# Optimization experiments

Hardware: AMD Instinct MI355X
Metric: run time of the kernel (lower is better)

Reference implementation:

```python
import jax, jax.numpy as jnp
import numpy as np

C = 16        # channel_n
HID = 128     # hidden width of 1x1 MLP
FIRE_RATE = 0.5
STEP_SIZE = 1.0
ALIVE_THRESH = 0.1
B, H, W = 16, 256, 256


def _perceive_kernel():
    # identity + Sobel filters, angle = 0.0 so cos=1, sin=0
    ident = np.outer([0.0, 1.0, 0.0], [0.0, 1.0, 0.0]).astype(np.float32)
    dxk = (np.outer([1.0, 2.0, 1.0], [-1.0, 0.0, 1.0]) / 8.0).astype(np.float32)
    dyk = dxk.T
    k3 = np.stack([ident, dxk, dyk], axis=-1)  # [3,3,3]
    # TF depthwise layout: out channel index = c*3 + k  -> tile over channels
    rhs = np.tile(k3, (1, 1, C)).reshape(3, 3, 1, 3 * C)  # HWIO, groups=C
    return jnp.asarray(rhs)


def _get_living_mask(x):
    alpha = x[:, :, :, 3:4]
    pooled = jax.lax.reduce_window(alpha, -jnp.inf, jax.lax.max,
                                   (1, 3, 3, 1), (1, 1, 1, 1), 'SAME')
    return pooled > ALIVE_THRESH


def _perceive(x):
    rhs = _perceive_kernel()
    return jax.lax.conv_general_dilated(
        x, rhs, window_strides=(1, 1), padding='SAME',
        dimension_numbers=('NHWC', 'HWIO', 'NHWC'),
        feature_group_count=C)  # [B,H,W,3C]


def setup_inputs() -> dict:
    key = jax.random.key(0)
    kx, kw1, kb1, ku = jax.random.split(key, 4)
    x = jax.random.normal(kx, (B, H, W, C), dtype=jnp.float32)
    # dmodel params: Conv2D(128,1,relu) then Conv2D(16,1,zeros init); use
    # random values for a meaningful numeric baseline
    W1 = jax.random.normal(kw1, (3 * C, HID), dtype=jnp.float32) * 0.1
    b1 = jax.random.normal(kb1, (HID,), dtype=jnp.float32) * 0.01
    W2 = jax.random.normal(jax.random.fold_in(key, 7), (HID, C), dtype=jnp.float32) * 0.1
    b2 = jnp.zeros((C,), dtype=jnp.float32)
    rand_u = jax.random.uniform(ku, (B, H, W, 1), dtype=jnp.float32)
    return {"x": x, "W1": W1, "b1": b1, "W2": W2, "b2": b2, "rand_u": rand_u}


def reference(x, W1, b1, W2, b2, rand_u):
    pre_life_mask = _get_living_mask(x)
    y = _perceive(x)                                         # [B,H,W,48]
    h = jax.nn.relu(jnp.einsum('bhwc,cd->bhwd', y, W1) + b1)  # [B,H,W,128]
    dx = (jnp.einsum('bhwd,dc->bhwc', h, W2) + b2) * STEP_SIZE
    update_mask = (rand_u <= FIRE_RATE).astype(x.dtype)
    x = x + dx * update_mask
    post_life_mask = _get_living_mask(x)
    life_mask = (pre_life_mask & post_life_mask).astype(x.dtype)
    return x * life_mask
```

## Files before the change

### kernel.cpp

```cpp
#include <hip/hip_runtime.h>


#define NB 16
#define NH 256
#define NW 256
#define NC 16
#define NHID 128
#define NPIX (NB*NH*NW)

__global__ __launch_bounds__(256) void ca_update(
    const float* __restrict__ x, const float* __restrict__ W1,
    const float* __restrict__ b1, const float* __restrict__ W2,
    const float* __restrict__ b2, const float* __restrict__ rand_u,
    float* __restrict__ out, float* __restrict__ ws_alpha, float* __restrict__ ws_pre)
{
    __shared__ float tile[18 * 18 * 17];

    const int tid = threadIdx.x;
    const int w0 = blockIdx.x * 16;
    const int h0 = blockIdx.y * 16;
    const int bb = blockIdx.z;

    for (int i = tid; i < 18 * 18; i += 256) {
        const int ly = i / 18, lx = i - ly * 18;
        const int gh = h0 + ly - 1, gw = w0 + lx - 1;
        float4 v0, v1, v2, v3;
        if (gh >= 0 && gh < NH && gw >= 0 && gw < NW) {
            const float4* p = (const float4*)(x + (((size_t)bb * NH + gh) * NW + gw) * NC);
            v0 = p[0]; v1 = p[1]; v2 = p[2]; v3 = p[3];
        } else {
            v0 = v1 = v2 = v3 = make_float4(0.f, 0.f, 0.f, 0.f);
        }
        float* t = &tile[i * 17];
        t[0]=v0.x; t[1]=v0.y; t[2]=v0.z; t[3]=v0.w;
        t[4]=v1.x; t[5]=v1.y; t[6]=v1.z; t[7]=v1.w;
        t[8]=v2.x; t[9]=v2.y; t[10]=v2.z; t[11]=v2.w;
        t[12]=v3.x; t[13]=v3.y; t[14]=v3.z; t[15]=v3.w;
    }
    __syncthreads();

    const int tx = tid & 15, ty = tid >> 4;
    const int lcc = ((ty + 1) * 18 + (tx + 1)) * 17;
    const int lmm = (ty * 18 + tx) * 17;
    const int lm0 = (ty * 18 + tx + 1) * 17;
    const int lmp = (ty * 18 + tx + 2) * 17;
    const int l0m = ((ty + 1) * 18 + tx) * 17;
    const int l0p = ((ty + 1) * 18 + tx + 2) * 17;
    const int lpm = ((ty + 2) * 18 + tx) * 17;
    const int lp0 = ((ty + 2) * 18 + tx + 1) * 17;
    const int lpp = ((ty + 2) * 18 + tx + 2) * 17;

    float y[48];
    #pragma unroll
    for (int c = 0; c < NC; ++c) {
        const float xmm = tile[lmm + c], xm0 = tile[lm0 + c], xmp = tile[lmp + c];
        const float x0m = tile[l0m + c], xcc = tile[lcc + c], x0p = tile[l0p + c];
        const float xpm = tile[lpm + c], xp0 = tile[lp0 + c], xpp = tile[lpp + c];
        y[3*c + 0] = xcc;
        y[3*c + 1] = ((xmp - xmm) + 2.f * (x0p - x0m) + (xpp - xpm)) * 0.125f;
        y[3*c + 2] = ((xpm - xmm) + 2.f * (xp0 - xm0) + (xpp - xmp)) * 0.125f;
    }

    float am = tile[lmm + 3];
    am = fmaxf(am, tile[lm0 + 3]); am = fmaxf(am, tile[lmp + 3]);
    am = fmaxf(am, tile[l0m + 3]); am = fmaxf(am, tile[lcc + 3]);
    am = fmaxf(am, tile[l0p + 3]);
    am = fmaxf(am, tile[lpm + 3]); am = fmaxf(am, tile[lp0 + 3]);
    am = fmaxf(am, tile[lpp + 3]);
    const float pre = (am > 0.1f) ? 1.f : 0.f;

    float dxacc[NC];
    #pragma unroll
    for (int c = 0; c < NC; ++c) dxacc[c] = b2[c];

    for (int d0 = 0; d0 < NHID; d0 += 4) {
        float a0 = b1[d0 + 0], a1 = b1[d0 + 1], a2 = b1[d0 + 2], a3 = b1[d0 + 3];
        #pragma unroll
        for (int c = 0; c < 48; ++c) {
            const float* wp = &W1[c * NHID + d0];
            const float yc = y[c];
            a0 = fmaf(yc, wp[0], a0);
            a1 = fmaf(yc, wp[1], a1);
            a2 = fmaf(yc, wp[2], a2);
            a3 = fmaf(yc, wp[3], a3);
        }
        a0 = fmaxf(a0, 0.f); a1 = fmaxf(a1, 0.f);
        a2 = fmaxf(a2, 0.f); a3 = fmaxf(a3, 0.f);
        const float* w2p = &W2[d0 * NC];
        #pragma unroll
        for (int c = 0; c < NC; ++c) {
            float t = fmaf(a0, w2p[c], dxacc[c]);
            t = fmaf(a1, w2p[NC + c], t);
            t = fmaf(a2, w2p[2 * NC + c], t);
            dxacc[c] = fmaf(a3, w2p[3 * NC + c], t);
        }
    }

    const size_t pix = ((size_t)bb * NH + (h0 + ty)) * NW + (w0 + tx);
    const float um = (rand_u[pix] <= 0.5f) ? 1.f : 0.f;
    float nx[NC];
    #pragma unroll
    for (int c = 0; c < NC; ++c) nx[c] = fmaf(dxacc[c], um, tile[lcc + c]);

    float4* po = (float4*)(out + pix * NC);
    po[0] = make_float4(nx[0], nx[1], nx[2], nx[3]);
    po[1] = make_float4(nx[4], nx[5], nx[6], nx[7]);
    po[2] = make_float4(nx[8], nx[9], nx[10], nx[11]);
    po[3] = make_float4(nx[12], nx[13], nx[14], nx[15]);
    ws_alpha[pix] = nx[3];
    ws_pre[pix] = pre;
}

__global__ __launch_bounds__(256) void ca_mask(
    const float* __restrict__ ws_alpha, const float* __restrict__ ws_pre,
    float* __restrict__ out)
{
    const size_t pix = (size_t)blockIdx.x * 256 + threadIdx.x;
    const int w = (int)(pix & 255);
    const int h = (int)((pix >> 8) & 255);
    const size_t base = pix - w - ((size_t)h << 8);

    float m = -1e30f;
    #pragma unroll
    for (int dy = -1; dy <= 1; ++dy) {
        const int hh = h + dy;
        if (hh < 0 || hh >= NH) continue;
        const size_t row = base + (size_t)hh * NW;
        #pragma unroll
        for (int dw = -1; dw <= 1; ++dw) {
            const int ww = w + dw;
            if (ww < 0 || ww >= NW) continue;
            m = fmaxf(m, ws_alpha[row + ww]);
        }
    }
    const bool life = (ws_pre[pix] != 0.f) && (m > 0.1f);
    const float s = life ? 1.f : 0.f;

    float4* po = (float4*)(out + pix * NC);
    #pragma unroll
    for (int i = 0; i < 4; ++i) {
        float4 v = po[i];
        v.x *= s; v.y *= s; v.z *= s; v.w *= s;
        po[i] = v;
    }
}

extern "C" void kernel_launch(void* const* d_in, const int* in_sizes, int n_in,
                              void* d_out, int out_size, void* d_ws, size_t ws_size,
                              hipStream_t stream) {
    (void)in_sizes; (void)n_in; (void)out_size; (void)ws_size;
    const float* x      = (const float*)d_in[0];
    const float* W1     = (const float*)d_in[1];
    const float* b1     = (const float*)d_in[2];
    const float* W2     = (const float*)d_in[3];
    const float* b2     = (const float*)d_in[4];
    const float* rand_u = (const float*)d_in[5];
    float* out = (float*)d_out;
    float* ws_alpha = (float*)d_ws;
    float* ws_pre   = ws_alpha + NPIX;

    dim3 gridA(NW / 16, NH / 16, NB);
    ca_update<<<gridA, 256, 0, stream>>>(x, W1, b1, W2, b2, rand_u, out, ws_alpha, ws_pre);
    ca_mask<<<NPIX / 256, 256, 0, stream>>>(ws_alpha, ws_pre, out);
}
```

Before: 391.2 us.

## Run the per-pixel MLP on bf16 MFMA with an exact fp32 recheck near the alive threshold

```diff
diff --git a/kernel.cpp b/kernel.cpp
--- a/kernel.cpp
+++ b/kernel.cpp
@@ -1,147 +1,292 @@
 #include <hip/hip_runtime.h>
 
 
-#define NB 16
-#define NH 256
-#define NW 256
 #define NC 16
 #define NHID 128
-#define NPIX (NB*NH*NW)
-
-__global__ __launch_bounds__(256) void ca_update(
+#define NPIX (16 * 256 * 256)
+#define MG 0.015f
+
+typedef __attribute__((ext_vector_type(8))) short s8b;
+typedef __attribute__((ext_vector_type(4))) float f4;
+
+__device__ __forceinline__ unsigned short f2bf(float f) {
+    union { float f; unsigned int u; } v; v.f = f;
+    unsigned int r = (v.u + 0x7FFFu + ((v.u >> 16) & 1u)) >> 16;
+    return (unsigned short)r;
+}
+__device__ __forceinline__ unsigned int pack2(float a, float b) {
+    return (unsigned int)f2bf(a) | ((unsigned int)f2bf(b) << 16);
+}
+
+__global__ __launch_bounds__(256) void ca_prep(
+    const float* __restrict__ W1, const float* __restrict__ b1,
+    const float* __restrict__ W2, uint4* __restrict__ w1p, uint4* __restrict__ w2p)
+{
+    const int tid = threadIdx.x;
+    if (blockIdx.x == 0) {
+        for (int idx = tid; idx < 1024; idx += 256) {
+            const int fid = idx >> 6, lane = idx & 63;
+            const int k0 = fid >> 3, mt = fid & 7;
+            const int q = lane >> 4, i = lane & 15;
+            unsigned int u[4];
+            #pragma unroll
+            for (int jp = 0; jp < 4; ++jp) {
+                int k = k0 * 32 + q * 8 + jp * 2;
+                float v0 = (k < 48) ? W1[k * 128 + mt * 16 + i] : ((k == 48) ? b1[mt * 16 + i] : 0.f);
+                k++;
+                float v1 = (k < 48) ? W1[k * 128 + mt * 16 + i] : ((k == 48) ? b1[mt * 16 + i] : 0.f);
+                u[jp] = pack2(v0, v1);
+            }
+            w1p[idx] = make_uint4(u[0], u[1], u[2], u[3]);
+        }
+    } else {
+        for (int idx = tid; idx < 256; idx += 256) {
+            const int k2 = idx >> 6, lane = idx & 63;
+            const int q = lane >> 4, i = lane & 15;
+            unsigned int u[4];
+            #pragma unroll
+            for (int jp = 0; jp < 4; ++jp) {
+                const int k = k2 * 32 + q * 8 + jp * 2;
+                u[jp] = pack2(W2[k * 16 + i], W2[(k + 1) * 16 + i]);
+            }
+            w2p[idx] = make_uint4(u[0], u[1], u[2], u[3]);
+        }
+    }
+}
+
+__global__ __launch_bounds__(256, 2) void ca_update(
+    const float* __restrict__ x, const float* __restrict__ b2,
+    const float* __restrict__ rand_u, const uint4* __restrict__ w1p,
+    const uint4* __restrict__ w2p, float* __restrict__ out,
+    float* __restrict__ ws_alpha, unsigned char* __restrict__ ws_pre)
+{
+    __shared__ __align__(16) float xt[18 * 18 * 20];
+    __shared__ __align__(16) unsigned short yfs[4 * 2 * 528];
+    __shared__ __align__(16) unsigned short hbs[4 * 16 * 136];
+    __shared__ float lsr[256];
+
+    const int tid  = threadIdx.x;
+    const int lane = tid & 63;
+    const int li   = lane & 15;
+    const int lq   = lane >> 4;
+    const int wv   = tid >> 6;
+    const int tx   = tid & 15, ty = tid >> 4;
+    const int w0 = blockIdx.x * 16, h0 = blockIdx.y * 16, bb = blockIdx.z;
+
+    s8b w1f[2][8], w2f[4];
+    const s8b* w1s = (const s8b*)w1p;
+    const s8b* w2s = (const s8b*)w2p;
+    #pragma unroll
+    for (int k0 = 0; k0 < 2; ++k0)
+        #pragma unroll
+        for (int mt = 0; mt < 8; ++mt)
+            w1f[k0][mt] = w1s[(k0 * 8 + mt) * 64 + lane];
+    #pragma unroll
+    for (int k2 = 0; k2 < 4; ++k2) w2f[k2] = w2s[k2 * 64 + lane];
+    float b2v[4];
+    #pragma unroll
+    for (int r = 0; r < 4; ++r) b2v[r] = b2[lq * 4 + r];
+
+    for (int i = tid; i < 324; i += 256) {
+        const int ly = i / 18, lx = i - ly * 18;
+        const int gh = h0 + ly - 1, gw = w0 + lx - 1;
+        float4 v0, v1, v2, v3;
+        if (gh >= 0 && gh < 256 && gw >= 0 && gw < 256) {
+            const float4* p = (const float4*)(x + (((size_t)bb * 256 + gh) * 256 + gw) * NC);
+            v0 = p[0]; v1 = p[1]; v2 = p[2]; v3 = p[3];
+        } else {
+            v0 = v1 = v2 = v3 = make_float4(0.f, 0.f, 0.f, 0.f);
+        }
+        float4* t = (float4*)(xt + i * 20);
+        t[0] = v0; t[1] = v1; t[2] = v2; t[3] = v3;
+    }
+    const size_t gpix = ((size_t)bb * 256 + h0 + ty) * 256 + (w0 + tx);
+    lsr[tid] = rand_u[gpix];
+    __syncthreads();
+
+    const int o_mm = ((ty + 0) * 18 + tx + 0) * 20, o_m0 = ((ty + 0) * 18 + tx + 1) * 20, o_mp = ((ty + 0) * 18 + tx + 2) * 20;
+    const int o_0m = ((ty + 1) * 18 + tx + 0) * 20, o_cc = ((ty + 1) * 18 + tx + 1) * 20, o_0p = ((ty + 1) * 18 + tx + 2) * 20;
+    const int o_pm = ((ty + 2) * 18 + tx + 0) * 20, o_p0 = ((ty + 2) * 18 + tx + 1) * 20, o_pp = ((ty + 2) * 18 + tx + 2) * 20;
+
+    float am = xt[o_mm + 3];
+    am = fmaxf(am, xt[o_m0 + 3]); am = fmaxf(am, xt[o_mp + 3]);
+    am = fmaxf(am, xt[o_0m + 3]); am = fmaxf(am, xt[o_cc + 3]); am = fmaxf(am, xt[o_0p + 3]);
+    am = fmaxf(am, xt[o_pm + 3]); am = fmaxf(am, xt[o_p0 + 3]); am = fmaxf(am, xt[o_pp + 3]);
+    ws_pre[gpix] = (am > 0.1f) ? (unsigned char)1 : (unsigned char)0;
+
+    unsigned int yu[24];
+    #pragma unroll
+    for (int cq = 0; cq < 4; ++cq) {
+        const int co = cq * 4;
+        float4 vmm = *(const float4*)(xt + o_mm + co); const float* pmm = (const float*)&vmm;
+        float4 vm0 = *(const float4*)(xt + o_m0 + co); const float* pm0 = (const float*)&vm0;
+        float4 vmp = *(const float4*)(xt + o_mp + co); const float* pmp = (const float*)&vmp;
+        float4 v0m = *(const float4*)(xt + o_0m + co); const float* p0m = (const float*)&v0m;
+        float4 vcc = *(const float4*)(xt + o_cc + co); const float* pcc = (const float*)&vcc;
+        float4 v0p = *(const float4*)(xt + o_0p + co); const float* p0p = (const float*)&v0p;
+        float4 vpm = *(const float4*)(xt + o_pm + co); const float* ppm = (const float*)&vpm;
+        float4 vp0 = *(const float4*)(xt + o_p0 + co); const float* pp0 = (const float*)&vp0;
+        float4 vpp = *(const float4*)(xt + o_pp + co); const float* ppp = (const float*)&vpp;
+        float yl[12];
+        #pragma unroll
+        for (int cc = 0; cc < 4; ++cc) {
+            const float xmm = pmm[cc], xm0 = pm0[cc], xmp = pmp[cc];
+            const float x0m = p0m[cc], xcc = pcc[cc], x0p = p0p[cc];
+            const float xpm = ppm[cc], xp0 = pp0[cc], xpp = ppp[cc];
+            yl[cc * 3 + 0] = xcc;
+            yl[cc * 3 + 1] = ((xmp - xmm) + 2.f * (x0p - x0m) + (xpp - xpm)) * 0.125f;
+            yl[cc * 3 + 2] = ((xpm - xmm) + 2.f * (xp0 - xm0) + (xpp - xmp)) * 0.125f;
+        }
+        #pragma unroll
+        for (int m2 = 0; m2 < 6; ++m2) yu[cq * 6 + m2] = pack2(yl[2 * m2], yl[2 * m2 + 1]);
+    }
+
+    unsigned short* yfw = yfs + wv * (2 * 528);
+    unsigned short* hbw = hbs + wv * (16 * 136);
+
+    for (int s = 0; s < 4; ++s) {
+        const int t = wv * 4 + s;
+        if ((ty & 3) == s) {
+            #pragma unroll
+            for (int q = 0; q < 4; ++q)
+                *(uint4*)(yfw + (q * 16 + tx) * 8) = make_uint4(yu[q * 4], yu[q * 4 + 1], yu[q * 4 + 2], yu[q * 4 + 3]);
+            *(uint4*)(yfw + 528 + (0 * 16 + tx) * 8) = make_uint4(yu[16], yu[17], yu[18], yu[19]);
+            *(uint4*)(yfw + 528 + (1 * 16 + tx) * 8) = make_uint4(yu[20], yu[21], yu[22], yu[23]);
+            *(uint4*)(yfw + 528 + (2 * 16 + tx) * 8) = make_uint4(0x3F80u, 0u, 0u, 0u);
+            *(uint4*)(yfw + 528 + (3 * 16 + tx) * 8) = make_uint4(0u, 0u, 0u, 0u);
+        }
+        __syncthreads();
+        const s8b ya0 = *(const s8b*)(yfw + lane * 8);
+        const s8b ya1 = *(const s8b*)(yfw + 528 + lane * 8);
+        f4 acc1[8];
+        #pragma unroll
+        for (int mt = 0; mt < 8; ++mt) { f4 z = {0.f, 0.f, 0.f, 0.f}; acc1[mt] = z; }
+        #pragma unroll
+        for (int mt = 0; mt < 8; ++mt)
+            acc1[mt] = __builtin_amdgcn_mfma_f32_16x16x32_bf16(w1f[0][mt], ya0, acc1[mt], 0, 0, 0);
+        #pragma unroll
+        for (int mt = 0; mt < 8; ++mt)
+            acc1[mt] = __builtin_amdgcn_mfma_f32_16x16x32_bf16(w1f[1][mt], ya1, acc1[mt], 0, 0, 0);
+        #pragma unroll
+        for (int mt = 0; mt < 8; ++mt) {
+            const float hh0 = fmaxf(acc1[mt][0], 0.f), hh1 = fmaxf(acc1[mt][1], 0.f);
+            const float hh2 = fmaxf(acc1[mt][2], 0.f), hh3 = fmaxf(acc1[mt][3], 0.f);
+            *(uint2*)(hbw + li * 136 + mt * 16 + lq * 4) = make_uint2(pack2(hh0, hh1), pack2(hh2, hh3));
+        }
+        __syncthreads();
+        f4 acc2 = {0.f, 0.f, 0.f, 0.f};
+        #pragma unroll
+        for (int k2 = 0; k2 < 4; ++k2) {
+            const s8b hf = *(const s8b*)(hbw + li * 136 + k2 * 32 + lq * 8);
+            acc2 = __builtin_amdgcn_mfma_f32_16x16x32_bf16(w2f[k2], hf, acc2, 0, 0, 0);
+        }
+        const float um = (lsr[t * 16 + li] <= 0.5f) ? 1.f : 0.f;
+        const float4 xc = *(const float4*)(xt + ((t + 1) * 18 + li + 1) * 20 + lq * 4);
+        float4 nx;
+        nx.x = fmaf(acc2[0] + b2v[0], um, xc.x);
+        nx.y = fmaf(acc2[1] + b2v[1], um, xc.y);
+        nx.z = fmaf(acc2[2] + b2v[2], um, xc.z);
+        nx.w = fmaf(acc2[3] + b2v[3], um, xc.w);
+        const size_t gp = ((size_t)bb * 256 + h0 + t) * 256 + (w0 + li);
+        ((float4*)out)[gp * 4 + lq] = nx;
+        if (lq == 0) ws_alpha[gp] = nx.w;
+    }
+}
+
+__device__ float exact_alpha(
     const float* __restrict__ x, const float* __restrict__ W1,
     const float* __restrict__ b1, const float* __restrict__ W2,
     const float* __restrict__ b2, const float* __restrict__ rand_u,
-    float* __restrict__ out, float* __restrict__ ws_alpha, float* __restrict__ ws_pre)
+    int bb, int gh, int gw)
 {
-    __shared__ float tile[18 * 18 * 17];
-
+    const size_t p = ((size_t)bb * 256 + gh) * 256 + gw;
+    const float xa = x[p * 16 + 3];
+    if (rand_u[p] > 0.5f) return xa;
+    float y[48];
+    #pragma unroll
+    for (int k = 0; k < 48; ++k) y[k] = 0.f;
+    for (int dy = 0; dy < 3; ++dy) {
+        for (int dx = 0; dx < 3; ++dx) {
+            const int hh = gh + dy - 1, ww = gw + dx - 1;
+            if (hh < 0 || hh >= 256 || ww < 0 || ww >= 256) continue;
+            const float* f = x + (((size_t)bb * 256 + hh) * 256 + ww) * 16;
+            const float rw = (dy == 1) ? 2.f : 1.f;
+            const float cw = (dx == 1) ? 2.f : 1.f;
+            const float wx = rw * (float)(dx - 1) * 0.125f;
+            const float wy = cw * (float)(dy - 1) * 0.125f;
+            const bool ctr = (dy == 1 && dx == 1);
+            #pragma unroll
+            for (int c = 0; c < 16; ++c) {
+                const float v = f[c];
+                if (ctr) y[3 * c] = v;
+                y[3 * c + 1] = fmaf(v, wx, y[3 * c + 1]);
+                y[3 * c + 2] = fmaf(v, wy, y[3 * c + 2]);
+            }
+        }
+    }
+    float dot = b2[3];
+    for (int d4 = 0; d4 < 32; ++d4) {
+        const float4 a4 = *(const float4*)(b1 + d4 * 4);
+        float a0 = a4.x, a1 = a4.y, a2 = a4.z, a3 = a4.w;
+        for (int k = 0; k < 48; ++k) {
+            const float4 w = *(const float4*)(W1 + k * 128 + d4 * 4);
+            const float yk = y[k];
+            a0 = fmaf(yk, w.x, a0); a1 = fmaf(yk, w.y, a1);
+            a2 = fmaf(yk, w.z, a2); a3 = fmaf(yk, w.w, a3);
+        }
+        dot = fmaf(fmaxf(a0, 0.f), W2[(d4 * 4 + 0) * 16 + 3], dot);
+        dot = fmaf(fmaxf(a1, 0.f), W2[(d4 * 4 + 1) * 16 + 3], dot);
+        dot = fmaf(fmaxf(a2, 0.f), W2[(d4 * 4 + 2) * 16 + 3], dot);
+        dot = fmaf(fmaxf(a3, 0.f), W2[(d4 * 4 + 3) * 16 + 3], dot);
+    }
+    return xa + dot;
+}
+
+__global__ __launch_bounds__(256) void ca_mask(
+    const float* __restrict__ x, const float* __restrict__ W1,
+    const float* __restrict__ b1, const float* __restrict__ W2,
+    const float* __restrict__ b2, const float* __restrict__ rand_u,
+    const float* __restrict__ alpha, const unsigned char* __restrict__ pre,
+    float* __restrict__ out)
+{
+    __shared__ float at[18 * 20];
     const int tid = threadIdx.x;
-    const int w0 = blockIdx.x * 16;
-    const int h0 = blockIdx.y * 16;
-    const int bb = blockIdx.z;
-
-    for (int i = tid; i < 18 * 18; i += 256) {
+    const int w0 = blockIdx.x * 16, h0 = blockIdx.y * 16, bb = blockIdx.z;
+    for (int i = tid; i < 324; i += 256) {
         const int ly = i / 18, lx = i - ly * 18;
         const int gh = h0 + ly - 1, gw = w0 + lx - 1;
-        float4 v0, v1, v2, v3;
-        if (gh >= 0 && gh < NH && gw >= 0 && gw < NW) {
-            const float4* p = (const float4*)(x + (((size_t)bb * NH + gh) * NW + gw) * NC);
-            v0 = p[0]; v1 = p[1]; v2 = p[2]; v3 = p[3];
-        } else {
-            v0 = v1 = v2 = v3 = make_float4(0.f, 0.f, 0.f, 0.f);
-        }
-        float* t = &tile[i * 17];
-        t[0]=v0.x; t[1]=v0.y; t[2]=v0.z; t[3]=v0.w;
-        t[4]=v1.x; t[5]=v1.y; t[6]=v1.z; t[7]=v1.w;
-        t[8]=v2.x; t[9]=v2.y; t[10]=v2.z; t[11]=v2.w;
-        t[12]=v3.x; t[13]=v3.y; t[14]=v3.z; t[15]=v3.w;
+        float v = 0.f;
+        if (gh >= 0 && gh < 256 && gw >= 0 && gw < 256)
+            v = alpha[((size_t)bb * 256 + gh) * 256 + gw];
+        at[ly * 20 + lx] = v;
     }
     __syncthreads();
-
-    const int tx = tid & 15, ty = tid >> 4;
-    const int lcc = ((ty + 1) * 18 + (tx + 1)) * 17;
-    const int lmm = (ty * 18 + tx) * 17;
-    const int lm0 = (ty * 18 + tx + 1) * 17;
-    const int lmp = (ty * 18 + tx + 2) * 17;
-    const int l0m = ((ty + 1) * 18 + tx) * 17;
-    const int l0p = ((ty + 1) * 18 + tx + 2) * 17;
-    const int lpm = ((ty + 2) * 18 + tx) * 17;
-    const int lp0 = ((ty + 2) * 18 + tx + 1) * 17;
-    const int lpp = ((ty + 2) * 18 + tx + 2) * 17;
-
-    float y[48];
-    #pragma unroll
-    for (int c = 0; c < NC; ++c) {
-        const float xmm = tile[lmm + c], xm0 = tile[lm0 + c], xmp = tile[lmp + c];
-        const float x0m = tile[l0m + c], xcc = tile[lcc + c], x0p = tile[l0p + c];
-        const float xpm = tile[lpm + c], xp0 = tile[lp0 + c], xpp = tile[lpp + c];
-        y[3*c + 0] = xcc;
-        y[3*c + 1] = ((xmp - xmm) + 2.f * (x0p - x0m) + (xpp - xpm)) * 0.125f;
-        y[3*c + 2] = ((xpm - xmm) + 2.f * (xp0 - xm0) + (xpp - xmp)) * 0.125f;
-    }
-
-    float am = tile[lmm + 3];
-    am = fmaxf(am, tile[lm0 + 3]); am = fmaxf(am, tile[lmp + 3]);
-    am = fmaxf(am, tile[l0m + 3]); am = fmaxf(am, tile[lcc + 3]);
-    am = fmaxf(am, tile[l0p + 3]);
-    am = fmaxf(am, tile[lpm + 3]); am = fmaxf(am, tile[lp0 + 3]);
-    am = fmaxf(am, tile[lpp + 3]);
-    const float pre = (am > 0.1f) ? 1.f : 0.f;
-
-    float dxacc[NC];
-    #pragma unroll
-    for (int c = 0; c < NC; ++c) dxacc[c] = b2[c];
-
-    for (int d0 = 0; d0 < NHID; d0 += 4) {
-        float a0 = b1[d0 + 0], a1 = b1[d0 + 1], a2 = b1[d0 + 2], a3 = b1[d0 + 3];
-        #pragma unroll
-        for (int c = 0; c < 48; ++c) {
-            const float* wp = &W1[c * NHID + d0];
-            const float yc = y[c];
-            a0 = fmaf(yc, wp[0], a0);
-            a1 = fmaf(yc, wp[1], a1);
-            a2 = fmaf(yc, wp[2], a2);
-            a3 = fmaf(yc, wp[3], a3);
-        }
-        a0 = fmaxf(a0, 0.f); a1 = fmaxf(a1, 0.f);
-        a2 = fmaxf(a2, 0.f); a3 = fmaxf(a3, 0.f);
-        const float* w2p = &W2[d0 * NC];
-        #pragma unroll
-        for (int c = 0; c < NC; ++c) {
-            float t = fmaf(a0, w2p[c], dxacc[c]);
-            t = fmaf(a1, w2p[NC + c], t);
-            t = fmaf(a2, w2p[2 * NC + c], t);
-            dxacc[c] = fmaf(a3, w2p[3 * NC + c], t);
-        }
-    }
-
-    const size_t pix = ((size_t)bb * NH + (h0 + ty)) * NW + (w0 + tx);
-    const float um = (rand_u[pix] <= 0.5f) ? 1.f : 0.f;
-    float nx[NC];
-    #pragma unroll
-    for (int c = 0; c < NC; ++c) nx[c] = fmaf(dxacc[c], um, tile[lcc + c]);
-
-    float4* po = (float4*)(out + pix * NC);
-    po[0] = make_float4(nx[0], nx[1], nx[2], nx[3]);
-    po[1] = make_float4(nx[4], nx[5], nx[6], nx[7]);
-    po[2] = make_float4(nx[8], nx[9], nx[10], nx[11]);
-    po[3] = make_float4(nx[12], nx[13], nx[14], nx[15]);
-    ws_alpha[pix] = nx[3];
-    ws_pre[pix] = pre;
-}
-
-__global__ __launch_bounds__(256) void ca_mask(
-    const float* __restrict__ ws_alpha, const float* __restrict__ ws_pre,
-    float* __restrict__ out)
-{
-    const size_t pix = (size_t)blockIdx.x * 256 + threadIdx.x;
-    const int w = (int)(pix & 255);
-    const int h = (int)((pix >> 8) & 255);
-    const size_t base = pix - w - ((size_t)h << 8);
-
-    float m = -1e30f;
-    #pragma unroll
-    for (int dy = -1; dy <= 1; ++dy) {
-        const int hh = h + dy;
-        if (hh < 0 || hh >= NH) continue;
-        const size_t row = base + (size_t)hh * NW;
-        #pragma unroll
-        for (int dw = -1; dw <= 1; ++dw) {
-            const int ww = w + dw;
-            if (ww < 0 || ww >= NW) continue;
-            m = fmaxf(m, ws_alpha[row + ww]);
-        }
-    }
-    const bool life = (ws_pre[pix] != 0.f) && (m > 0.1f);
-    const float s = life ? 1.f : 0.f;
-
-    float4* po = (float4*)(out + pix * NC);
-    #pragma unroll
-    for (int i = 0; i < 4; ++i) {
-        float4 v = po[i];
-        v.x *= s; v.y *= s; v.z *= s; v.w *= s;
-        po[i] = v;
+    const int txx = tid & 15, tyy = tid >> 4;
+    float m = at[tyy * 20 + txx];
+    m = fmaxf(m, at[tyy * 20 + txx + 1]); m = fmaxf(m, at[tyy * 20 + txx + 2]);
+    m = fmaxf(m, at[(tyy + 1) * 20 + txx]); m = fmaxf(m, at[(tyy + 1) * 20 + txx + 1]); m = fmaxf(m, at[(tyy + 1) * 20 + txx + 2]);
+    m = fmaxf(m, at[(tyy + 2) * 20 + txx]); m = fmaxf(m, at[(tyy + 2) * 20 + txx + 1]); m = fmaxf(m, at[(tyy + 2) * 20 + txx + 2]);
+    bool alive;
+    if (m > 0.1f + MG) alive = true;
+    else if (m <= 0.1f - MG) alive = false;
+    else {
+        alive = false;
+        for (int nb = 0; nb < 9; ++nb) {
+            if (alive) break;
+            const int dy = nb / 3, dx = nb - dy * 3;
+            const float a = at[(tyy + dy) * 20 + txx + dx];
+            if (a > 0.1f - MG) {
+                const float tr = exact_alpha(x, W1, b1, W2, b2, rand_u, bb, h0 + tyy + dy - 1, w0 + txx + dx - 1);
+                if (tr > 0.1f) alive = true;
+            }
+        }
+    }
+    const size_t gp = ((size_t)bb * 256 + h0 + tyy) * 256 + (w0 + txx);
+    const float sc = (alive && pre[gp]) ? 1.f : 0.f;
+    float4* po = (float4*)(out + gp * 16);
+    #pragma unroll
+    for (int i2 = 0; i2 < 4; ++i2) {
+        float4 v = po[i2]; v.x *= sc; v.y *= sc; v.z *= sc; v.w *= sc; po[i2] = v;
     }
 }
 
@@ -149,17 +294,20 @@
                               void* d_out, int out_size, void* d_ws, size_t ws_size,
                               hipStream_t stream) {
     (void)in_sizes; (void)n_in; (void)out_size; (void)ws_size;
-    const float* x      = (const float*)d_in[0];
-    const float* W1     = (const float*)d_in[1];
-    const float* b1     = (const float*)d_in[2];
-    const float* W2     = (const float*)d_in[3];
-    const float* b2     = (const float*)d_in[4];
-    const float* rand_u = (const float*)d_in[5];
+    const float* x  = (const float*)d_in[0];
+    const float* W1 = (const float*)d_in[1];
+    const float* b1 = (const float*)d_in[2];
+    const float* W2 = (const float*)d_in[3];
+    const float* b2 = (const float*)d_in[4];
+    const float* ru = (const float*)d_in[5];
     float* out = (float*)d_out;
     float* ws_alpha = (float*)d_ws;
-    float* ws_pre   = ws_alpha + NPIX;
-
-    dim3 gridA(NW / 16, NH / 16, NB);
-    ca_update<<<gridA, 256, 0, stream>>>(x, W1, b1, W2, b2, rand_u, out, ws_alpha, ws_pre);
-    ca_mask<<<NPIX / 256, 256, 0, stream>>>(ws_alpha, ws_pre, out);
-}
+    unsigned char* ws_pre = (unsigned char*)(ws_alpha + NPIX);
+    uint4* w1p = (uint4*)((char*)d_ws + (size_t)NPIX * 5);
+    uint4* w2p = w1p + 1024;
+
+    ca_prep<<<2, 256, 0, stream>>>(W1, b1, W2, w1p, w2p);
+    dim3 g(16, 16, 16);
+    ca_update<<<g, 256, 0, stream>>>(x, b2, ru, w1p, w2p, out, ws_alpha, ws_pre);
+    ca_mask<<<g, 256, 0, stream>>>(x, W1, b1, W2, b2, ru, ws_alpha, ws_pre, out);
+}
```

Measured after the change: 340.0 us. 13.1% less time.
